# Optimization experiments

Measured on AMD Instinct MI355X. Metric: run time of the kernel, lower is better.

Reference implementation:

```python
import jax, jax.numpy as jnp
import numpy as np

TOPK = 20
EPS = 1e-5  # torch BatchNorm1d default eps


def _segment_softmax(logits, seg, num_segments):
    m = jax.ops.segment_max(logits, seg, num_segments=num_segments)
    e = jnp.exp(logits - m[seg])
    s = jax.ops.segment_sum(e, seg, num_segments=num_segments)
    return e / (s[seg] + 1e-16)


def _forward(data, emb, W_lin, att_i, att_j, att_em_i, att_em_j, bias_gnn,
             W_ff, b_ff, bn1_g, bn1_b, bn2_g, bn2_b, W_out, b_out):
    B, N, F = data.shape
    H, D = att_i.shape
    BN = B * N
    x = data.reshape(BN, F)

    # --- dynamic top-k cosine-similarity graph (original detaches embeddings) ---
    w = jax.lax.stop_gradient(emb)
    nrm = jnp.linalg.norm(w, axis=-1, keepdims=True)  # (N,1)
    cos = (w @ w.T) / (nrm * nrm.T)                   # (N,N)
    _, topk_idx = jax.lax.top_k(cos, TOPK)            # (N,K)

    src = topk_idx.reshape(-1)                        # j (source of message)
    tgt = jnp.repeat(jnp.arange(N), TOPK)             # i (target)
    off = (jnp.arange(B) * N)[:, None]                # batch the edge list
    src_b = (src[None, :] + off).reshape(-1)          # (B*N*K,)
    tgt_b = (tgt[None, :] + off).reshape(-1)
    # remove_self_loops then add_self_loops: mask topk self-edges, append loops
    self_mask = src_b == tgt_b
    loops = jnp.arange(BN)
    src_all = jnp.concatenate([src_b, loops])         # (E,)
    tgt_all = jnp.concatenate([tgt_b, loops])
    dead = jnp.concatenate([self_mask, jnp.zeros(BN, dtype=bool)])

    # --- GraphLayer: GAT-style attention with node embeddings in the keys ---
    xh = (x @ W_lin).reshape(BN, H, D)                # lin(x), per head
    emb_full = jnp.tile(emb, (B, 1))                  # (BN, D) repeated per batch
    # per-node attention scores; key_i = [x_i || emb_i] . [att_i || att_em_i]
    score_i = jnp.einsum('nhd,hd->nh', xh, att_i) + emb_full @ att_em_i.T  # (BN,H)
    score_j = jnp.einsum('nhd,hd->nh', xh, att_j) + emb_full @ att_em_j.T
    alpha = score_i[tgt_all] + score_j[src_all]       # (E,H)
    alpha = jax.nn.leaky_relu(alpha, 0.2)
    alpha = jnp.where(dead[:, None], -1e30, alpha)    # drop removed self-edges
    alpha = _segment_softmax(alpha, tgt_all, BN)      # softmax over in-edges of i
    msgs = xh[src_all] * alpha[:, :, None]            # (E,H,D)
    agg = jax.ops.segment_sum(msgs, tgt_all, num_segments=BN)  # (BN,H,D)
    out = agg.reshape(BN, H * D) + bias_gnn           # concat heads + bias

    # --- GNNLayer head: linear -> BatchNorm1d (train stats) -> relu ---
    out = out @ W_ff + b_ff                           # (BN, D)
    mu = out.mean(0)
    var = out.var(0)
    out = (out - mu) / jnp.sqrt(var + EPS) * bn1_g + bn1_b
    out = jax.nn.relu(out)

    # --- multiply by embeddings, channelwise BN, relu (dropout: eval = identity) ---
    h = out.reshape(B, N, D) * emb[None]              # (B,N,D)
    mu2 = h.mean(axis=(0, 1))
    var2 = h.var(axis=(0, 1))
    h = (h - mu2) / jnp.sqrt(var2 + EPS) * bn2_g + bn2_b
    h = jax.nn.relu(h)

    # --- OutLayer (layer_num=1): single linear per node ---
    return h @ W_out + b_out                          # (B, N, out_win)


def setup_inputs() -> dict:
    key = jax.random.key(0)
    ks = jax.random.split(key, 12)
    B, N, F, D, H, OW = 16, 2000, 128, 64, 4, 200
    s = 0.05
    return {
        'data': jax.random.normal(ks[0], (B, N, F), jnp.float32),
        'emb': jax.random.normal(ks[1], (N, D), jnp.float32),
        'W_lin': jax.random.normal(ks[2], (F, H * D), jnp.float32) * s,
        'att_i': jax.random.normal(ks[3], (H, D), jnp.float32) * s,
        'att_j': jax.random.normal(ks[4], (H, D), jnp.float32) * s,
        'att_em_i': jax.random.normal(ks[5], (H, D), jnp.float32) * s,
        'att_em_j': jax.random.normal(ks[6], (H, D), jnp.float32) * s,
        'bias_gnn': jnp.zeros((H * D,), jnp.float32),
        'W_ff': jax.random.normal(ks[7], (H * D, D), jnp.float32) * s,
        'b_ff': jnp.zeros((D,), jnp.float32),
        'bn1_g': jnp.ones((D,), jnp.float32),
        'bn1_b': jnp.zeros((D,), jnp.float32),
        'bn2_g': jnp.ones((D,), jnp.float32),
        'bn2_b': jnp.zeros((D,), jnp.float32),
        'W_out': jax.random.normal(ks[8], (D, OW), jnp.float32) * s,
        'b_out': jnp.zeros((OW,), jnp.float32),
    }


def reference(data, emb, W_lin, att_i, att_j, att_em_i, att_em_j, bias_gnn,
              W_ff, b_ff, bn1_g, bn1_b, bn2_g, bn2_b, W_out, b_out):
    return _forward(data, emb, W_lin, att_i, att_j, att_em_i, att_em_j, bias_gnn,
                    W_ff, b_ff, bn1_g, bn1_b, bn2_g, bn2_b, W_out, b_out)
```

## Files before the change

### kernel.cpp

```cpp
#include <hip/hip_runtime.h>
#include <math.h>

#define B_   16
#define N_   2000
#define F_   128
#define D_   64
#define H_   4
#define OW_  200
#define K_   20
#define BN_  (B_*N_)
#define HD_  (H_*D_)
#define EPS_ 1e-5f
#define NP_  2048

__global__ __launch_bounds__(256) void k_prep(const float* __restrict__ emb,
                                              const float* __restrict__ Wlin,
                                              const float* __restrict__ atti,
                                              const float* __restrict__ attj,
                                              const float* __restrict__ attei,
                                              const float* __restrict__ attej,
                                              const float* __restrict__ biasg,
                                              const float* __restrict__ Wff,
                                              const float* __restrict__ bff,
                                              float* __restrict__ nrm,
                                              float* __restrict__ embT,
                                              float* __restrict__ W2,
                                              float* __restrict__ wscore,
                                              float* __restrict__ semb,
                                              float* __restrict__ bias2) {
    const int t = threadIdx.x, b = blockIdx.x;
    if (b < 512) {
        const int idx = b * 256 + t;
        int k = idx >> 11, j = idx & (NP_ - 1);
        embT[idx] = (j < N_) ? emb[(size_t)j * D_ + k] : 0.f;
        if (b < 8) {
            int i = idx;
            if (i < N_) {
                const float* e = emb + (size_t)i * D_;
                float s = 0.f;
                #pragma unroll
                for (int d = 0; d < D_; ++d) s += e[d] * e[d];
                nrm[i] = sqrtf(s);
            } else if (i < NP_) {
                nrm[i] = 1.f;
            }
        }
    } else if (b < 640) {
        const int f = b - 512;
        const int h = t >> 6, d = t & 63;
        float s = 0.f;
        for (int dd = 0; dd < D_; ++dd)
            s = fmaf(Wlin[(size_t)f * HD_ + h * D_ + dd],
                     Wff[(size_t)(h * D_ + dd) * D_ + d], s);
        W2[(size_t)f * HD_ + t] = s;
    } else if (b < 644) {
        const int idx = (b - 640) * 256 + t;
        const int f = idx >> 3, c8 = idx & 7;
        const int h = c8 & 3;
        const float* a = (c8 < 4) ? atti : attj;
        float s = 0.f;
        for (int d = 0; d < D_; ++d)
            s = fmaf(Wlin[(size_t)f * HD_ + h * D_ + d], a[h * D_ + d], s);
        wscore[idx] = s;
    } else if (b < 707) {
        const int idx = (b - 644) * 256 + t;
        const int i = idx >> 3, c8 = idx & 7;
        if (i < N_) {
            const int h = c8 & 3;
            const float* a = (c8 < 4) ? attei : attej;
            float s = 0.f;
            for (int d = 0; d < D_; ++d)
                s = fmaf(emb[(size_t)i * D_ + d], a[h * D_ + d], s);
            semb[idx] = s;
        }
    } else {
        if (t < D_) {
            float s = bff[t];
            for (int c = 0; c < HD_; ++c)
                s = fmaf(biasg[c], Wff[(size_t)c * D_ + t], s);
            bias2[t] = s;
        }
    }
}

__global__ __launch_bounds__(256) void k_cos(const float* __restrict__ emb,
                                             const float* __restrict__ embT,
                                             const float* __restrict__ nrm,
                                             float* __restrict__ cosm) {
    const int t    = threadIdx.x;
    const int i0   = blockIdx.y * 16;
    const int r0   = (t >> 6) * 4;
    const int lane = t & 63;
    const int j4   = blockIdx.x * 256 + lane * 4;

    __shared__ float eL[16 * D_];
    for (int idx = t; idx < 16 * D_; idx += 256)
        eL[idx] = emb[(size_t)i0 * D_ + idx];
    __syncthreads();

    float acc[4][4];
    #pragma unroll
    for (int r = 0; r < 4; ++r)
        #pragma unroll
        for (int cc = 0; cc < 4; ++cc) acc[r][cc] = 0.f;

    for (int k4 = 0; k4 < D_; k4 += 4) {
        float es[4][4];
        #pragma unroll
        for (int r = 0; r < 4; ++r) {
            float4 ev = *(const float4*)&eL[(r0 + r) * D_ + k4];
            es[r][0] = ev.x; es[r][1] = ev.y; es[r][2] = ev.z; es[r][3] = ev.w;
        }
        #pragma unroll
        for (int kk = 0; kk < 4; ++kk) {
            float4 b = *(const float4*)&embT[(size_t)(k4 + kk) * NP_ + j4];
            #pragma unroll
            for (int r = 0; r < 4; ++r) {
                acc[r][0] = fmaf(es[r][kk], b.x, acc[r][0]);
                acc[r][1] = fmaf(es[r][kk], b.y, acc[r][1]);
                acc[r][2] = fmaf(es[r][kk], b.z, acc[r][2]);
                acc[r][3] = fmaf(es[r][kk], b.w, acc[r][3]);
            }
        }
    }

    float4 nj = *(const float4*)&nrm[j4];
    #pragma unroll
    for (int r = 0; r < 4; ++r) {
        float ni = nrm[i0 + r0 + r];
        float4 o;
        o.x = acc[r][0] / (ni * nj.x);
        o.y = acc[r][1] / (ni * nj.y);
        o.z = acc[r][2] / (ni * nj.z);
        o.w = acc[r][3] / (ni * nj.w);
        *(float4*)&cosm[(size_t)(i0 + r0 + r) * NP_ + j4] = o;
    }
}

__device__ __forceinline__ unsigned long long kmax64(unsigned long long a,
                                                     unsigned long long b) {
    return a > b ? a : b;
}

__global__ __launch_bounds__(256) void k_sel(const float* __restrict__ cosm,
                                             int* __restrict__ topk) {
    const int t    = threadIdx.x;
    const int lane = t & 63;
    const int i    = blockIdx.x * 4 + (t >> 6);
    const float* row = cosm + (size_t)i * NP_;

    unsigned long long key[32];
    #pragma unroll
    for (int m = 0; m < 8; ++m) {
        float4 b = *(const float4*)&row[m * 256 + lane * 4];
        float vv[4] = {b.x, b.y, b.z, b.w};
        #pragma unroll
        for (int q = 0; q < 4; ++q) {
            const int s = m * 4 + q;
            const int j = m * 256 + lane * 4 + q;
            unsigned int x  = __float_as_uint(vv[q]);
            unsigned int mv = (x & 0x80000000u) ? ~x : (x | 0x80000000u);
            unsigned long long kk =
                ((unsigned long long)mv << 32) | (unsigned int)(NP_ - 1 - j);
            key[s] = (j < N_) ? kk : 0ull;
        }
    }

    unsigned long long loc;
    {
        unsigned long long l1[16];
        #pragma unroll
        for (int s = 0; s < 16; ++s) l1[s] = kmax64(key[s], key[s + 16]);
        unsigned long long l2[8];
        #pragma unroll
        for (int s = 0; s < 8; ++s) l2[s] = kmax64(l1[s], l1[s + 8]);
        unsigned long long l3[4];
        #pragma unroll
        for (int s = 0; s < 4; ++s) l3[s] = kmax64(l2[s], l2[s + 4]);
        loc = kmax64(kmax64(l3[0], l3[2]), kmax64(l3[1], l3[3]));
    }

    for (int k = 0; k < K_; ++k) {
        unsigned long long w = loc;
        #pragma unroll
        for (int off = 1; off < 64; off <<= 1)
            w = kmax64(w, __shfl_xor(w, off, 64));

        if (lane == 0)
            topk[i * K_ + k] = (NP_ - 1) - (int)(unsigned int)(w & 0xFFFFFFFFu);

        #pragma unroll
        for (int s = 0; s < 32; ++s)
            if (key[s] == w) key[s] = 0ull;
        {
            unsigned long long l1[16];
            #pragma unroll
            for (int s = 0; s < 16; ++s) l1[s] = kmax64(key[s], key[s + 16]);
            unsigned long long l2[8];
            #pragma unroll
            for (int s = 0; s < 8; ++s) l2[s] = kmax64(l1[s], l1[s + 8]);
            unsigned long long l3[4];
            #pragma unroll
            for (int s = 0; s < 4; ++s) l3[s] = kmax64(l2[s], l2[s + 4]);
            loc = kmax64(kmax64(l3[0], l3[2]), kmax64(l3[1], l3[3]));
        }
    }
}

#define XS_ 132
__global__ __launch_bounds__(256) void k_lin(const float* __restrict__ x,
                                             const float* __restrict__ W2,
                                             const float* __restrict__ wscore,
                                             const float* __restrict__ semb,
                                             float* __restrict__ yh,
                                             float* __restrict__ si,
                                             float* __restrict__ sj) {
    const int t    = threadIdx.x;
    const int n0   = blockIdx.x * 32;
    const int r0   = (t >> 6) * 8;
    const int lane = t & 63;
    const int c4   = lane * 4;

    __shared__ float xL[32 * XS_];
    __shared__ float wsL[F_ * 8];

    for (int idx = t; idx < 32 * F_; idx += 256)
        xL[(idx >> 7) * XS_ + (idx & 127)] = x[(size_t)n0 * F_ + idx];
    for (int idx = t; idx < F_ * 8; idx += 256)
        wsL[idx] = wscore[idx];
    __syncthreads();

    float acc[8][4];
    #pragma unroll
    for (int r = 0; r < 8; ++r)
        #pragma unroll
        for (int cc = 0; cc < 4; ++cc) acc[r][cc] = 0.f;

    for (int k4 = 0; k4 < F_; k4 += 4) {
        float xs[8][4];
        #pragma unroll
        for (int r = 0; r < 8; ++r) {
            float4 xv = *(const float4*)&xL[(r0 + r) * XS_ + k4];
            xs[r][0] = xv.x; xs[r][1] = xv.y; xs[r][2] = xv.z; xs[r][3] = xv.w;
        }
        #pragma unroll
        for (int kk = 0; kk < 4; ++kk) {
            float4 w = *(const float4*)&W2[(size_t)(k4 + kk) * HD_ + c4];
            #pragma unroll
            for (int r = 0; r < 8; ++r) {
                acc[r][0] = fmaf(xs[r][kk], w.x, acc[r][0]);
                acc[r][1] = fmaf(xs[r][kk], w.y, acc[r][1]);
                acc[r][2] = fmaf(xs[r][kk], w.z, acc[r][2]);
                acc[r][3] = fmaf(xs[r][kk], w.w, acc[r][3]);
            }
        }
    }

    #pragma unroll
    for (int r = 0; r < 8; ++r) {
        float4 o; o.x = acc[r][0]; o.y = acc[r][1]; o.z = acc[r][2]; o.w = acc[r][3];
        *(float4*)&yh[(size_t)(n0 + r0 + r) * HD_ + c4] = o;
    }

    {
        const int row = t >> 3, c8 = t & 7;
        float s = 0.f;
        for (int k4 = 0; k4 < F_; k4 += 4) {
            float4 xv = *(const float4*)&xL[row * XS_ + k4];
            s = fmaf(xv.x, wsL[(k4 + 0) * 8 + c8], s);
            s = fmaf(xv.y, wsL[(k4 + 1) * 8 + c8], s);
            s = fmaf(xv.z, wsL[(k4 + 2) * 8 + c8], s);
            s = fmaf(xv.w, wsL[(k4 + 3) * 8 + c8], s);
        }
        const int n = n0 + row;
        const int i = n % N_;
        s += semb[i * 8 + c8];
        if (c8 < 4) si[(size_t)n * H_ + c8]       = s;
        else        sj[(size_t)n * H_ + (c8 - 4)] = s;
    }
}

#define RA_ 8
__global__ __launch_bounds__(256) void k_attn(const float* __restrict__ yh,
                                              const float* __restrict__ si,
                                              const float* __restrict__ sj,
                                              const int* __restrict__ topk,
                                              const float* __restrict__ bias2,
                                              float* __restrict__ out2) {
    const int t   = threadIdx.x;
    const int nwg = BN_ / RA_;
    const int swz = (blockIdx.x & 7) * (nwg >> 3) + (blockIdx.x >> 3);
    const int n0  = swz * RA_;
    __shared__ int   srcL[RA_][21];
    __shared__ float wA[RA_][H_][21];

    if (t < RA_ * 21) {
        const int r = t / 21, e = t % 21;
        const int n = n0 + r;
        const int i = n % N_;
        const int b = n / N_;
        int s; bool dead = false;
        if (e < K_) { int kk = topk[i * K_ + e]; s = b * N_ + kk; dead = (kk == i); }
        else        { s = n; }
        srcL[r][e] = s;
        #pragma unroll
        for (int h = 0; h < H_; ++h) {
            float a = si[(size_t)n * H_ + h] + sj[(size_t)s * H_ + h];
            a = a > 0.f ? a : 0.2f * a;
            if (dead) a = -1e30f;
            wA[r][h][e] = a;
        }
    }
    __syncthreads();

    if (t < RA_ * H_) {
        const int r = t >> 2, h = t & 3;
        float m = -3e38f;
        for (int e = 0; e < 21; ++e) m = fmaxf(m, wA[r][h][e]);
        float sum = 0.f;
        for (int e = 0; e < 21; ++e) { float ex = expf(wA[r][h][e] - m); wA[r][h][e] = ex; sum += ex; }
        float inv = 1.f / (sum + 1e-16f);
        for (int e = 0; e < 21; ++e) wA[r][h][e] *= inv;
    }
    __syncthreads();

    {
        const int g = t >> 6, lane = t & 63, c4 = lane * 4, h = lane >> 4;
        #pragma unroll
        for (int rr = 0; rr < 2; ++rr) {
            const int r = g * 2 + rr;
            float a0 = 0.f, a1 = 0.f, a2 = 0.f, a3 = 0.f;
            for (int e = 0; e < 21; ++e) {
                float wv = wA[r][h][e];
                float4 yv = *(const float4*)&yh[(size_t)srcL[r][e] * HD_ + c4];
                a0 = fmaf(wv, yv.x, a0); a1 = fmaf(wv, yv.y, a1);
                a2 = fmaf(wv, yv.z, a2); a3 = fmaf(wv, yv.w, a3);
            }
            a0 += __shfl_xor(a0, 16); a0 += __shfl_xor(a0, 32);
            a1 += __shfl_xor(a1, 16); a1 += __shfl_xor(a1, 32);
            a2 += __shfl_xor(a2, 16); a2 += __shfl_xor(a2, 32);
            a3 += __shfl_xor(a3, 16); a3 += __shfl_xor(a3, 32);
            if (lane < 16) {
                float4 b2 = *(const float4*)&bias2[lane * 4];
                float4 o; o.x = a0 + b2.x; o.y = a1 + b2.y;
                          o.z = a2 + b2.z; o.w = a3 + b2.w;
                *(float4*)&out2[(size_t)(n0 + r) * D_ + lane * 4] = o;
            }
        }
    }
}

__global__ __launch_bounds__(256) void k_red1(const float* __restrict__ out2,
                                              double* __restrict__ S,
                                              double* __restrict__ SS) {
    const int t = threadIdx.x;
    double s = 0.0, ss = 0.0;
    const int total = BN_ * D_;
    for (int idx = blockIdx.x * 256 + t; idx < total; idx += gridDim.x * 256) {
        float v = out2[idx];
        s += v; ss += (double)v * v;
    }
    __shared__ double sb[256], ssb[256];
    sb[t] = s; ssb[t] = ss;
    __syncthreads();
    if (t < 64) {
        double a = sb[t] + sb[t + 64] + sb[t + 128] + sb[t + 192];
        double b = ssb[t] + ssb[t + 64] + ssb[t + 128] + ssb[t + 192];
        atomicAdd(&S[t], a);
        atomicAdd(&SS[t], b);
    }
}

__global__ __launch_bounds__(256) void k_bn1(const float* __restrict__ out2,
                                             const float* __restrict__ emb,
                                             const double* __restrict__ S1,
                                             const double* __restrict__ SS1,
                                             const float* __restrict__ g1,
                                             const float* __restrict__ b1,
                                             float* __restrict__ hb,
                                             double* __restrict__ S2,
                                             double* __restrict__ SS2) {
    const int t = threadIdx.x;
    __shared__ float scale[64], shift[64];
    if (t < 64) {
        double mu  = S1[t] / (double)BN_;
        double var = SS1[t] / (double)BN_ - mu * mu;
        float rstd = rsqrtf((float)var + EPS_);
        float sc   = rstd * g1[t];
        scale[t] = sc;
        shift[t] = b1[t] - (float)mu * sc;
    }
    __syncthreads();
    const int d = t & 63;
    double s = 0.0, ss = 0.0;
    const int total = BN_ * D_;
    for (int idx = blockIdx.x * 256 + t; idx < total; idx += gridDim.x * 256) {
        float v = out2[idx];
        v = v * scale[d] + shift[d];
        v = fmaxf(v, 0.f);
        int n = idx >> 6;
        int i = n % N_;
        v *= emb[(size_t)i * D_ + d];
        hb[idx] = v;
        s += v; ss += (double)v * v;
    }
    __shared__ double sb[256], ssb[256];
    sb[t] = s; ssb[t] = ss;
    __syncthreads();
    if (t < 64) {
        double a = sb[t] + sb[t + 64] + sb[t + 128] + sb[t + 192];
        double b = ssb[t] + ssb[t + 64] + ssb[t + 128] + ssb[t + 192];
        atomicAdd(&S2[t], a);
        atomicAdd(&SS2[t], b);
    }
}

__global__ __launch_bounds__(256) void k_out(const float* __restrict__ hb,
                                             const double* __restrict__ S2,
                                             const double* __restrict__ SS2,
                                             const float* __restrict__ g2,
                                             const float* __restrict__ b2,
                                             const float* __restrict__ Wout,
                                             const float* __restrict__ bout,
                                             float* __restrict__ out) {
    const int t  = threadIdx.x;
    const int n0 = blockIdx.x * 16;
    __shared__ float scale[64], shift[64];
    __shared__ float hL[16 * D_];
    if (t < 64) {
        double mu  = S2[t] / (double)BN_;
        double var = SS2[t] / (double)BN_ - mu * mu;
        float rstd = rsqrtf((float)var + EPS_);
        float sc   = rstd * g2[t];
        scale[t] = sc;
        shift[t] = b2[t] - (float)mu * sc;
    }
    __syncthreads();
    for (int idx = t; idx < 16 * D_; idx += 256) {
        float v = hb[(size_t)n0 * D_ + idx];
        int d = idx & 63;
        v = fmaxf(v * scale[d] + shift[d], 0.f);
        hL[idx] = v;
    }
    __syncthreads();
    if (t < OW_) {
        float acc[16];
        #pragma unroll
        for (int r = 0; r < 16; ++r) acc[r] = 0.f;
        for (int d4 = 0; d4 < D_; d4 += 4) {
            float hs[16][4];
            #pragma unroll
            for (int r = 0; r < 16; ++r) {
                float4 hv = *(const float4*)&hL[r * D_ + d4];
                hs[r][0] = hv.x; hs[r][1] = hv.y; hs[r][2] = hv.z; hs[r][3] = hv.w;
            }
            #pragma unroll
            for (int kk = 0; kk < 4; ++kk) {
                float w = Wout[(size_t)(d4 + kk) * OW_ + t];
                #pragma unroll
                for (int r = 0; r < 16; ++r) acc[r] = fmaf(hs[r][kk], w, acc[r]);
            }
        }
        float bo = bout[t];
        #pragma unroll
        for (int r = 0; r < 16; ++r) out[(size_t)(n0 + r) * OW_ + t] = acc[r] + bo;
    }
}

extern "C" void kernel_launch(void* const* d_in, const int* in_sizes, int n_in,
                              void* d_out, int out_size, void* d_ws, size_t ws_size,
                              hipStream_t stream) {
    const float* data  = (const float*)d_in[0];
    const float* emb   = (const float*)d_in[1];
    const float* Wlin  = (const float*)d_in[2];
    const float* atti  = (const float*)d_in[3];
    const float* attj  = (const float*)d_in[4];
    const float* attei = (const float*)d_in[5];
    const float* attej = (const float*)d_in[6];
    const float* biasg = (const float*)d_in[7];
    const float* Wff   = (const float*)d_in[8];
    const float* bff   = (const float*)d_in[9];
    const float* g1    = (const float*)d_in[10];
    const float* b1    = (const float*)d_in[11];
    const float* g2    = (const float*)d_in[12];
    const float* b2    = (const float*)d_in[13];
    const float* Wout  = (const float*)d_in[14];
    const float* bout  = (const float*)d_in[15];
    float* out = (float*)d_out;

    char* w = (char*)d_ws;
    size_t off = 0;
    auto alloc = [&](size_t bytes) -> void* {
        void* p = w + off;
        off += (bytes + 255) & ~(size_t)255;
        return p;
    };
    float*  nrm    = (float*) alloc((size_t)NP_ * sizeof(float));
    int*    topk   = (int*)   alloc((size_t)N_ * K_ * sizeof(int));
    float*  bias2  = (float*) alloc((size_t)D_ * sizeof(float));
    float*  W2     = (float*) alloc((size_t)F_ * HD_ * sizeof(float));
    float*  wscore = (float*) alloc((size_t)F_ * 8 * sizeof(float));
    float*  semb   = (float*) alloc((size_t)N_ * 8 * sizeof(float));
    float*  yh   = (float*) alloc((size_t)BN_ * HD_ * sizeof(float));
    float*  embT = yh;
    float*  cosm = yh + (size_t)D_ * NP_;
    float*  si   = (float*) alloc((size_t)BN_ * H_ * sizeof(float));
    float*  sj   = (float*) alloc((size_t)BN_ * H_ * sizeof(float));
    float*  out2 = (float*) alloc((size_t)BN_ * D_ * sizeof(float));
    float*  hb   = (float*) alloc((size_t)BN_ * D_ * sizeof(float));
    double* S1   = (double*)alloc(64 * sizeof(double));
    double* SS1  = (double*)alloc(64 * sizeof(double));
    double* S2   = (double*)alloc(64 * sizeof(double));
    double* SS2  = (double*)alloc(64 * sizeof(double));

    hipMemsetAsync(S1, 0, 4 * 512, stream);

    hipLaunchKernelGGL(k_prep,  dim3(708),          dim3(256), 0, stream,
                       emb, Wlin, atti, attj, attei, attej, biasg, Wff, bff,
                       nrm, embT, W2, wscore, semb, bias2);
    hipLaunchKernelGGL(k_cos,   dim3(NP_/256, N_/16), dim3(256), 0, stream,
                       emb, embT, nrm, cosm);
    hipLaunchKernelGGL(k_sel,   dim3(N_/4),          dim3(256), 0, stream, cosm, topk);
    hipLaunchKernelGGL(k_lin,   dim3(BN_ / 32),      dim3(256), 0, stream,
                       data, W2, wscore, semb, yh, si, sj);
    hipLaunchKernelGGL(k_attn,  dim3(BN_ / RA_),     dim3(256), 0, stream,
                       yh, si, sj, topk, bias2, out2);
    hipLaunchKernelGGL(k_red1,  dim3(512),           dim3(256), 0, stream, out2, S1, SS1);
    hipLaunchKernelGGL(k_bn1,   dim3(512),           dim3(256), 0, stream,
                       out2, emb, S1, SS1, g1, b1, hb, S2, SS2);
    hipLaunchKernelGGL(k_out,   dim3(BN_ / 16),      dim3(256), 0, stream,
                       hb, S2, SS2, g2, b2, Wout, bout, out);
}
```

Before: 262.9 us.

## Fuse BN1 statistics reduction into attention kernel and drop memset

The first batch-norm sum and sum-of-squares reduction is folded into the attention kernel. Each block stages its output rows in shared memory and issues per-channel double atomics, so the separate k_red1 pass that re-read out2 from global memory goes away. Rows per block go from 8 to 16 to halve the number of atomics, and the accumulator zeroing moves from hipMemsetAsync into k_prep, which removes one launch. The cost is more atomic traffic on 64 addresses from the 2000 attention blocks and half as many blocks available for latency hiding.

```diff
diff --git a/kernel.cpp b/kernel.cpp
--- a/kernel.cpp
+++ b/kernel.cpp
@@ -27,7 +27,11 @@
                                               float* __restrict__ W2,
                                               float* __restrict__ wscore,
                                               float* __restrict__ semb,
-                                              float* __restrict__ bias2) {
+                                              float* __restrict__ bias2,
+                                              double* __restrict__ S1,
+                                              double* __restrict__ SS1,
+                                              double* __restrict__ S2,
+                                              double* __restrict__ SS2) {
     const int t = threadIdx.x, b = blockIdx.x;
     if (b < 512) {
         const int idx = b * 256 + t;
@@ -79,6 +83,7 @@
             for (int c = 0; c < HD_; ++c)
                 s = fmaf(biasg[c], Wff[(size_t)c * D_ + t], s);
             bias2[t] = s;
+            S1[t] = 0.0; SS1[t] = 0.0; S2[t] = 0.0; SS2[t] = 0.0;
         }
     }
 }
@@ -280,22 +285,25 @@
     }
 }
 
-#define RA_ 8
+#define RA_ 16
 __global__ __launch_bounds__(256) void k_attn(const float* __restrict__ yh,
                                               const float* __restrict__ si,
                                               const float* __restrict__ sj,
                                               const int* __restrict__ topk,
                                               const float* __restrict__ bias2,
-                                              float* __restrict__ out2) {
+                                              float* __restrict__ out2,
+                                              double* __restrict__ S1,
+                                              double* __restrict__ SS1) {
     const int t   = threadIdx.x;
     const int nwg = BN_ / RA_;
     const int swz = (blockIdx.x & 7) * (nwg >> 3) + (blockIdx.x >> 3);
     const int n0  = swz * RA_;
     __shared__ int   srcL[RA_][21];
     __shared__ float wA[RA_][H_][21];
-
-    if (t < RA_ * 21) {
-        const int r = t / 21, e = t % 21;
+    __shared__ float oL[RA_][D_];
+
+    for (int idx = t; idx < RA_ * 21; idx += 256) {
+        const int r = idx / 21, e = idx % 21;
         const int n = n0 + r;
         const int i = n % N_;
         const int b = n / N_;
@@ -327,8 +335,8 @@
     {
         const int g = t >> 6, lane = t & 63, c4 = lane * 4, h = lane >> 4;
         #pragma unroll
-        for (int rr = 0; rr < 2; ++rr) {
-            const int r = g * 2 + rr;
+        for (int rr = 0; rr < 4; ++rr) {
+            const int r = g * 4 + rr;
             float a0 = 0.f, a1 = 0.f, a2 = 0.f, a3 = 0.f;
             for (int e = 0; e < 21; ++e) {
                 float wv = wA[r][h][e];
@@ -345,29 +353,21 @@
                 float4 o; o.x = a0 + b2.x; o.y = a1 + b2.y;
                           o.z = a2 + b2.z; o.w = a3 + b2.w;
                 *(float4*)&out2[(size_t)(n0 + r) * D_ + lane * 4] = o;
-            }
-        }
-    }
-}
-
-__global__ __launch_bounds__(256) void k_red1(const float* __restrict__ out2,
-                                              double* __restrict__ S,
-                                              double* __restrict__ SS) {
-    const int t = threadIdx.x;
-    double s = 0.0, ss = 0.0;
-    const int total = BN_ * D_;
-    for (int idx = blockIdx.x * 256 + t; idx < total; idx += gridDim.x * 256) {
-        float v = out2[idx];
-        s += v; ss += (double)v * v;
-    }
-    __shared__ double sb[256], ssb[256];
-    sb[t] = s; ssb[t] = ss;
-    __syncthreads();
-    if (t < 64) {
-        double a = sb[t] + sb[t + 64] + sb[t + 128] + sb[t + 192];
-        double b = ssb[t] + ssb[t + 64] + ssb[t + 128] + ssb[t + 192];
-        atomicAdd(&S[t], a);
-        atomicAdd(&SS[t], b);
+                *(float4*)&oL[r][lane * 4] = o;
+            }
+        }
+    }
+    __syncthreads();
+
+    if (t < D_) {
+        double s = 0.0, ss = 0.0;
+        #pragma unroll
+        for (int r = 0; r < RA_; ++r) {
+            double v = (double)oL[r][t];
+            s += v; ss += v * v;
+        }
+        atomicAdd(&S1[t], s);
+        atomicAdd(&SS1[t], ss);
     }
 }
 
@@ -513,19 +513,16 @@
     double* S2   = (double*)alloc(64 * sizeof(double));
     double* SS2  = (double*)alloc(64 * sizeof(double));
 
-    hipMemsetAsync(S1, 0, 4 * 512, stream);
-
     hipLaunchKernelGGL(k_prep,  dim3(708),          dim3(256), 0, stream,
                        emb, Wlin, atti, attj, attei, attej, biasg, Wff, bff,
-                       nrm, embT, W2, wscore, semb, bias2);
+                       nrm, embT, W2, wscore, semb, bias2, S1, SS1, S2, SS2);
     hipLaunchKernelGGL(k_cos,   dim3(NP_/256, N_/16), dim3(256), 0, stream,
                        emb, embT, nrm, cosm);
     hipLaunchKernelGGL(k_sel,   dim3(N_/4),          dim3(256), 0, stream, cosm, topk);
     hipLaunchKernelGGL(k_lin,   dim3(BN_ / 32),      dim3(256), 0, stream,
                        data, W2, wscore, semb, yh, si, sj);
     hipLaunchKernelGGL(k_attn,  dim3(BN_ / RA_),     dim3(256), 0, stream,
-                       yh, si, sj, topk, bias2, out2);
-    hipLaunchKernelGGL(k_red1,  dim3(512),           dim3(256), 0, stream, out2, S1, SS1);
+                       yh, si, sj, topk, bias2, out2, S1, SS1);
     hipLaunchKernelGGL(k_bn1,   dim3(512),           dim3(256), 0, stream,
                        out2, emb, S1, SS1, g1, b1, hb, S2, SS2);
     hipLaunchKernelGGL(k_out,   dim3(BN_ / 16),      dim3(256), 0, stream,
```

Result: slower. 280.3 us (+6.6%).
